# Kernel optimization log

Hardware: AMD Instinct MI355X
Metric: run time of the kernel (lower is better)

Reference implementation:

```python
import jax, jax.numpy as jnp
import numpy as np

S, L, E = 64, 256, 768          # sentences, tokens per sentence, BERT hidden
N, P = 4096, 32768              # events, event pairs
C, H, D = 256, 4, 64            # CGE channels, heads, head dim (C = H*D = n_last)
M = 8                           # max event span length
MLP_H = 1024
ITERS = 3                       # max_iteration + 1
RATE = 0.5
BETA_INTRA, BETA_INTER = 0.5, 0.5


def setup_inputs():
    key = jax.random.key(0)
    ks = jax.random.split(key, 16)
    nrm = lambda k, shape, sc: jax.random.normal(k, shape, dtype=jnp.float32) * sc
    event_start = jax.random.randint(ks[2], (N,), 0, L - M)
    span = jax.random.randint(ks[3], (N,), 1, M + 1)
    return {
        "sent_emb": nrm(ks[0], (S, L, E), 1.0),
        "proj_in_W": nrm(ks[7], (E, C), E ** -0.5),
        "proj_in_b": jnp.zeros((C,), jnp.float32),
        "proj_W": nrm(ks[8], (C, C), C ** -0.5),
        "proj_b": jnp.zeros((C,), jnp.float32),
        "att_src_intra": nrm(ks[9], (H, D), D ** -0.5),
        "att_dst_intra": nrm(ks[10], (H, D), D ** -0.5),
        "att_src_inter": nrm(ks[11], (H, D), D ** -0.5),
        "att_dst_inter": nrm(ks[12], (H, D), D ** -0.5),
        "mlp_W1": nrm(ks[13], (C + 2 * E, MLP_H), (C + 2 * E) ** -0.5),
        "mlp_b1": jnp.zeros((MLP_H,), jnp.float32),
        "mlp_W2": nrm(ks[14], (MLP_H, 3), MLP_H ** -0.5),
        "mlp_b2": jnp.zeros((3,), jnp.float32),
        "event_sent": jax.random.randint(ks[1], (N,), 0, S),
        "event_start": event_start,
        "event_end": event_start + span,
        "pair_idx": jax.random.randint(ks[4], (P, 2), 0, N),
        "rel_type": jax.random.randint(ks[5], (P,), 0, 2),
        "target": jax.random.randint(ks[6], (P,), 0, 3),
    }


def _attend(h, src, dst, emask, att_src, att_dst):
    # h: [N,H,D]. Masked graph attention, softmax over incoming edges per dst.
    a = jax.nn.leaky_relu((h[src] * att_src).sum(-1) + (h[dst] * att_dst).sum(-1), 0.2)  # [En,H]
    a = jnp.where(emask[:, None], a, -1e9)
    amax = jnp.maximum(jax.ops.segment_max(a, dst, num_segments=N), -1e9)  # [N,H]
    ex = jnp.exp(a - amax[dst]) * emask[:, None].astype(a.dtype)
    denom = jax.ops.segment_sum(ex, dst, num_segments=N)
    alpha = ex / (denom[dst] + 1e-9)
    out = jax.ops.segment_sum(alpha[:, :, None] * h[src], dst, num_segments=N)  # [N,H,D]
    return out.reshape(N, H * D)


def _forward(sent_emb, proj_in_W, proj_in_b, proj_W, proj_b,
             att_src_intra, att_dst_intra, att_src_inter, att_dst_inter,
             mlp_W1, mlp_b1, mlp_W2, mlp_b2,
             event_sent, event_start, event_end, pair_idx, rel_type, target):
    # extract_event: mean of sentence token embeddings over each event span
    pos = event_start[:, None] + jnp.arange(M)                      # [N,M]
    vmask = (pos < event_end[:, None]).astype(sent_emb.dtype)       # [N,M]
    tok = sent_emb[event_sent[:, None], jnp.clip(pos, 0, L - 1)]    # [N,M,E]
    e_emb = (tok * vmask[..., None]).sum(1) / (event_end - event_start).astype(sent_emb.dtype)[:, None]

    p0, p1 = pair_idx[:, 0], pair_idx[:, 1]
    pair_emb = jnp.concatenate([e_emb[p0], e_emb[p1]], axis=-1)     # [P,2E]
    x = e_emb @ proj_in_W + proj_in_b                               # [N,C]

    self_idx = jnp.arange(N)
    ones_n = jnp.ones((N,), bool)
    src_all = jnp.concatenate([p0, p1])
    dst_all = jnp.concatenate([p1, p0])
    intra2 = jnp.concatenate([rel_type == 0, rel_type == 0])

    loss = jnp.float32(0.0)
    pred = None
    for it in range(ITERS):
        diff = x[p0] - x[p1]                                        # [P,C]
        pre = jnp.concatenate([pair_emb, diff], axis=-1)            # [P,2E+C]
        pred = jax.nn.relu(pre @ mlp_W1 + mlp_b1) @ mlp_W2 + mlp_b2  # [P,3]
        logp = jax.nn.log_softmax(pred, axis=-1)
        loss = loss + (1.0 / (it + 1)) * (-jnp.take_along_axis(logp, target[:, None], axis=1).mean())

        # data-dependent edge construction (masked, fixed-size edge lists)
        psoft = jax.nn.softmax(pred, axis=-1)
        conf = psoft.max(1) > RATE
        parg = psoft.argmax(1)
        m_all = jnp.concatenate([conf & (parg == 1), conf & (parg == 2)])

        h = (x @ proj_W + proj_b).reshape(N, H, D)
        # intra edges + always-on self loops
        src_i = jnp.concatenate([src_all, self_idx])
        dst_i = jnp.concatenate([dst_all, self_idx])
        m_i = jnp.concatenate([m_all & intra2, ones_n])
        out_intra = _attend(h, src_i, dst_i, m_i, att_src_intra, att_dst_intra)
        out_inter = _attend(h, src_all, dst_all, m_all & (~intra2), att_src_inter, att_dst_inter)
        x = BETA_INTRA * out_intra + BETA_INTER * out_inter
    return loss, pred


def reference(sent_emb, proj_in_W, proj_in_b, proj_W, proj_b,
              att_src_intra, att_dst_intra, att_src_inter, att_dst_inter,
              mlp_W1, mlp_b1, mlp_W2, mlp_b2,
              event_sent, event_start, event_end, pair_idx, rel_type, target):
    return _forward(sent_emb, proj_in_W, proj_in_b, proj_W, proj_b,
                    att_src_intra, att_dst_intra, att_src_inter, att_dst_inter,
                    mlp_W1, mlp_b1, mlp_W2, mlp_b2,
                    event_sent, event_start, event_end, pair_idx, rel_type, target)
```

## Files before the change

kernel.cpp:

```cpp
#include <hip/hip_runtime.h>
#include <cstddef>
#include <cstdint>

#define NEV   4096
#define NPAIR 32768
#define NEDGE (2*NPAIR)
#define EDIM  768
#define CDIM  256
#define MLPH  1024
#define LLEN  256

typedef unsigned short u16;
typedef __attribute__((ext_vector_type(8))) short bhalf8;
typedef __attribute__((ext_vector_type(4))) float f32x4;

#define GLOAD_LDS(g, l) __builtin_amdgcn_global_load_lds( \
    (const __attribute__((address_space(1))) unsigned int*)(g), \
    (__attribute__((address_space(3))) unsigned int*)(l), 16, 0, 0)

__device__ inline u16 f2bf(float f) {
  union { float f; unsigned u; } v; v.f = f;
  unsigned r = v.u + 0x7fffu + ((v.u >> 16) & 1u);
  return (u16)(r >> 16);
}
__device__ inline float bf2f(u16 h) {
  union { unsigned u; float f; } v; v.u = ((unsigned)h) << 16; return v.f;
}

__global__ void k_zero(int* __restrict__ deg, int* __restrict__ pdeg,
                       float* __restrict__ out) {
  int i = blockIdx.x * 256 + threadIdx.x;
  if (i < NEV) { deg[i] = 0; pdeg[i] = 0; }
  if (i == 0) out[0] = 0.f;
}

__global__ void k_embed(const float* __restrict__ sent, const int* __restrict__ es,
                        const int* __restrict__ st, const int* __restrict__ en,
                        u16* __restrict__ Ahat) {
  int node = blockIdx.x;
  int s = es[node];
  int a = st[node];
  int span = en[node] - a;
  float fspan = (float)span;
  const float* base = sent + ((size_t)s * LLEN + a) * EDIM;
  for (int d = threadIdx.x; d < EDIM; d += 256) {
    float acc = 0.f;
    for (int m = 0; m < span; ++m) acc += base[(size_t)m * EDIM + d];
    float e = acc / fspan;
    u16 hi = f2bf(e);
    float lo = e - bf2f(hi);
    size_t b = (size_t)node * (3 * EDIM);
    Ahat[b + d] = hi;
    Ahat[b + EDIM + d] = hi;
    Ahat[b + 2 * EDIM + d] = f2bf(lo);
  }
}

__global__ void k_countF(const int* __restrict__ pair, int* __restrict__ deg,
                         int* __restrict__ pdeg) {
  int e = blockIdx.x * 256 + threadIdx.x;
  if (e >= NEDGE) return;
  int p = (e < NPAIR) ? e : e - NPAIR;
  int dst = (e < NPAIR) ? pair[2 * p + 1] : pair[2 * p];
  atomicAdd(&deg[dst], 1);
  if (e < NPAIR) atomicAdd(&pdeg[pair[2 * e]], 1);
}

__device__ inline void scan_body(const int* __restrict__ deg, int* __restrict__ rowp,
                                 int* __restrict__ cursor, int* part) {
  int t = threadIdx.x;
  int base = t * 16;
  int sum = 0;
  for (int i = 0; i < 16; ++i) sum += deg[base + i];
  part[t] = sum;
  __syncthreads();
  for (int off = 1; off < 256; off <<= 1) {
    int v = (t >= off) ? part[t - off] : 0;
    __syncthreads();
    part[t] += v;
    __syncthreads();
  }
  int run = (t == 0) ? 0 : part[t - 1];
  for (int i = 0; i < 16; ++i) {
    rowp[base + i] = run;
    cursor[base + i] = 0;
    run += deg[base + i];
  }
  if (t == 255) rowp[NEV] = run;
}

__global__ void k_scanF(const int* __restrict__ deg, int* __restrict__ rowp,
                        int* __restrict__ cursor, const int* __restrict__ pdeg,
                        int* __restrict__ prow, int* __restrict__ pcur) {
  __shared__ int part[256];
  scan_body(deg, rowp, cursor, part);
  __syncthreads();
  scan_body(pdeg, prow, pcur, part);
}

__global__ void k_scatterF(const int* __restrict__ pair, const int* __restrict__ rowp,
                           int* __restrict__ cursor, int* __restrict__ e_src,
                           int* __restrict__ e_id, const int* __restrict__ prow,
                           int* __restrict__ pcur, int* __restrict__ pidx) {
  int e = blockIdx.x * 256 + threadIdx.x;
  if (e >= NEDGE) return;
  int p   = (e < NPAIR) ? e : e - NPAIR;
  int src = (e < NPAIR) ? pair[2 * p]     : pair[2 * p + 1];
  int dst = (e < NPAIR) ? pair[2 * p + 1] : pair[2 * p];
  int pos = rowp[dst] + atomicAdd(&cursor[dst], 1);
  e_src[pos] = src;
  e_id[pos]  = e;
  if (e < NPAIR) {
    int pp = prow[pair[2 * e]] + atomicAdd(&pcur[pair[2 * e]], 1);
    pidx[pp] = e;
  }
}

__global__ __launch_bounds__(256) void cvt_w(const float* __restrict__ W1,
                                             const float* __restrict__ piW,
                                             const float* __restrict__ projW,
                                             u16* __restrict__ BTe,
                                             u16* __restrict__ BTu)
{
  __shared__ float tile[32][33];
  int which = (blockIdx.y >= 24) ? 1 : 0;
  if (which && blockIdx.x >= 40) return;
  u16* BT = which ? BTu : BTe;
  int K = which ? CDIM : EDIM;
  int ld = K * 3;
  int bk = (which ? (blockIdx.y - 24) : blockIdx.y) * 32;
  int bc = blockIdx.x * 32;
  int tx = threadIdx.x & 31, ty = threadIdx.x >> 5;
#pragma unroll
  for (int rr = 0; rr < 4; ++rr) {
    int k = bk + ty + rr * 8;
    int c = bc + tx;
    float v;
    if (which == 0) {
      v = (c < 1024) ? W1[(size_t)k * MLPH + c]
        : (c < 2048) ? W1[(size_t)(EDIM + k) * MLPH + (c - 1024)]
        : piW[(size_t)k * CDIM + (c - 2048)];
    } else {
      v = (c < 1024) ? W1[(size_t)(2 * EDIM + k) * MLPH + c]
        : projW[(size_t)k * CDIM + (c - 1024)];
    }
    tile[ty + rr * 8][tx] = v;
  }
  __syncthreads();
#pragma unroll
  for (int rr = 0; rr < 4; ++rr) {
    int c = bc + ty + rr * 8;
    int k = bk + tx;
    float v = tile[tx][ty + rr * 8];
    u16 hi = f2bf(v);
    float lo = v - bf2f(hi);
    size_t b = (size_t)c * ld;
    BT[b + k] = hi;
    BT[b + K + k] = f2bf(lo);
    BT[b + 2 * K + k] = hi;
  }
}

__global__ __launch_bounds__(256) void mgemm(
    const u16* __restrict__ A, const u16* __restrict__ BT, int Kp, int mode,
    float* __restrict__ G1, float* __restrict__ G2, u16* __restrict__ Xhat,
    const float* __restrict__ pib, const float* __restrict__ b1,
    const float* __restrict__ pb, float* __restrict__ U, float* __restrict__ V,
    float* __restrict__ h, const float* __restrict__ asi,
    const float* __restrict__ adi, const float* __restrict__ asj,
    const float* __restrict__ adj, float* __restrict__ sv)
{
  __shared__ u16 As[64 * 64];
  __shared__ u16 Bs[128 * 64];
  int tid = threadIdx.x;
  int wave = tid >> 6, lane = tid & 63;

  int gx = gridDim.x;
  int nwg = gx * gridDim.y;
  int orig = blockIdx.y * gx + blockIdx.x;
  int swz = (orig & 7) * (nwg >> 3) + (orig >> 3);
  int bm = (swz / gx) * 64, bn = (swz % gx) * 128;

  int wm = (wave >> 1) * 32, wn = (wave & 1) * 64;

  int srow = tid >> 3;
  int scol = (tid & 7) << 3;
  const u16* Ag = A + (size_t)(bm + srow) * Kp + scol;
  const u16* Bg = BT + (size_t)(bn + srow) * Kp + scol;
  u16* Asd = &As[tid * 8];
  u16* Bsd = &Bs[tid * 8];

  f32x4 acc[2][4];
#pragma unroll
  for (int i = 0; i < 2; ++i)
#pragma unroll
    for (int j = 0; j < 4; ++j) {
      f32x4 z = {0.f, 0.f, 0.f, 0.f};
      acc[i][j] = z;
    }

  int fr = lane & 15;
  int fq = lane >> 4;

  for (int k0 = 0; k0 < Kp; k0 += 64) {
#pragma unroll
    for (int c = 0; c < 2; ++c)
      GLOAD_LDS(Ag + (size_t)(c * 32) * Kp, Asd + c * 2048);
#pragma unroll
    for (int c = 0; c < 4; ++c)
      GLOAD_LDS(Bg + (size_t)(c * 32) * Kp, Bsd + c * 2048);
    __syncthreads();
#pragma unroll
    for (int kk = 0; kk < 2; ++kk) {
      bhalf8 af[2], bf[4];
#pragma unroll
      for (int i = 0; i < 2; ++i)
        af[i] = *(const bhalf8*)&As[(wm + i * 16 + fr) * 64 + kk * 32 + fq * 8];
#pragma unroll
      for (int j = 0; j < 4; ++j)
        bf[j] = *(const bhalf8*)&Bs[(wn + j * 16 + fr) * 64 + kk * 32 + fq * 8];
#pragma unroll
      for (int i = 0; i < 2; ++i)
#pragma unroll
        for (int j = 0; j < 4; ++j)
          acc[i][j] = __builtin_amdgcn_mfma_f32_16x16x32_bf16(af[i], bf[j], acc[i][j], 0, 0, 0);
    }
    __syncthreads();
    Ag += 64;
    Bg += 64;
  }

#pragma unroll
  for (int i = 0; i < 2; ++i) {
    int mrow = bm + wm + i * 16 + fq * 4;
#pragma unroll
    for (int g = 0; g < 4; ++g) {
      int m = mrow + g;
#pragma unroll
      for (int j = 0; j < 4; ++j) {
        int c = bn + wn + j * 16 + fr;
        float vv = acc[i][j][g];
        if (mode == 0) {
          if (c < 1024) {
            G1[(size_t)m * MLPH + c] = vv;
          } else if (c < 2048) {
            G2[(size_t)m * MLPH + (c - 1024)] = vv;
          } else {
            int cc = c - 2048;
            float xv = vv + pib[cc];
            u16 hi = f2bf(xv);
            float lo = xv - bf2f(hi);
            size_t b = (size_t)m * (3 * CDIM);
            Xhat[b + cc] = hi;
            Xhat[b + CDIM + cc] = hi;
            Xhat[b + 2 * CDIM + cc] = f2bf(lo);
          }
        } else {
          if (c < 1024) {
            size_t idx = (size_t)m * MLPH + c;
            U[idx] = G1[idx] + vv + b1[c];
            V[idx] = G2[idx] - vv;
          } else {
            int cc = c - 1024;
            h[(size_t)m * CDIM + cc] = vv + pb[cc];
          }
        }
      }
    }
  }

  if (mode == 1 && bn >= MLPH) {
    int hbase = bn - MLPH + wn;
    int head = hbase >> 6;
#pragma unroll
    for (int i = 0; i < 2; ++i) {
#pragma unroll
      for (int g = 0; g < 4; ++g) {
        int m = bm + wm + i * 16 + fq * 4 + g;
        float p0 = 0.f, p1 = 0.f, p2 = 0.f, p3 = 0.f;
#pragma unroll
        for (int j = 0; j < 4; ++j) {
          int hc = hbase + j * 16 + fr;
          float hv = acc[i][j][g] + pb[hc];
          p0 += hv * asi[hc];
          p1 += hv * adi[hc];
          p2 += hv * asj[hc];
          p3 += hv * adj[hc];
        }
#pragma unroll
        for (int mm = 1; mm < 16; mm <<= 1) {
          p0 += __shfl_xor(p0, mm);
          p1 += __shfl_xor(p1, mm);
          p2 += __shfl_xor(p2, mm);
          p3 += __shfl_xor(p3, mm);
        }
        if (fr == 0) {
          sv[0 * NEV * 4 + m * 4 + head] = p0;
          sv[1 * NEV * 4 + m * 4 + head] = p1;
          sv[2 * NEV * 4 + m * 4 + head] = p2;
          sv[3 * NEV * 4 + m * 4 + head] = p3;
        }
      }
    }
  }
}

__global__ __launch_bounds__(256) void k_pred_g(
    const float* __restrict__ U, const float* __restrict__ V,
    const int* __restrict__ pair, const int* __restrict__ prow,
    const int* __restrict__ pidx, const float* __restrict__ W2,
    const float* __restrict__ b2, const int* __restrict__ target,
    int* __restrict__ mstate, float* __restrict__ out,
    float* __restrict__ partials, float lossCoef)
{
  __shared__ float ush[MLPH];
  __shared__ float red[4];
  int n = blockIdx.x;
  int tid = threadIdx.x;
  const float* u = U + (size_t)n * MLPH;
#pragma unroll
  for (int i = 0; i < 4; ++i) ush[tid + i * 256] = u[tid + i * 256];
  __syncthreads();
  int wv = tid >> 6, lane = tid & 63;
  int beg = prow[n], end = prow[n + 1];
  float lsum = 0.f;
  for (int ip = beg + wv; ip < end; ip += 4) {
    int p = pidx[ip];
    int i1 = pair[2 * p + 1];
    const float* v = V + (size_t)i1 * MLPH;
    float a0 = 0.f, a1 = 0.f, a2 = 0.f;
    for (int kb = (lane << 2); kb < MLPH; kb += 256) {
      float4 uu = *(const float4*)(&ush[kb]);
      float4 vv = *(const float4*)(v + kb);
      float h0 = fmaxf(uu.x + vv.x, 0.f);
      float h1 = fmaxf(uu.y + vv.y, 0.f);
      float h2 = fmaxf(uu.z + vv.z, 0.f);
      float h3 = fmaxf(uu.w + vv.w, 0.f);
      const float4* w4 = (const float4*)(W2 + 3 * kb);
      float4 wa = w4[0], wb = w4[1], wc = w4[2];
      a0 += h0 * wa.x + h1 * wa.w + h2 * wb.z + h3 * wc.y;
      a1 += h0 * wa.y + h1 * wb.x + h2 * wb.w + h3 * wc.z;
      a2 += h0 * wa.z + h1 * wb.y + h2 * wc.x + h3 * wc.w;
    }
#pragma unroll
    for (int m = 32; m >= 1; m >>= 1) {
      a0 += __shfl_down(a0, m);
      a1 += __shfl_down(a1, m);
      a2 += __shfl_down(a2, m);
    }
    if (lane == 0) {
      a0 += b2[0]; a1 += b2[1]; a2 += b2[2];
      float mx = fmaxf(a0, fmaxf(a1, a2));
      float e0 = expf(a0 - mx), e1 = expf(a1 - mx), e2 = expf(a2 - mx);
      float sum = e0 + e1 + e2;
      int arg = 0; float best = e0;
      if (e1 > best) { best = e1; arg = 1; }
      if (e2 > best) { best = e2; arg = 2; }
      bool conf = (best / sum) > 0.5f;
      mstate[p] = conf ? arg : -1;
      int t = target[p];
      float predt = (t == 0) ? a0 : ((t == 1) ? a1 : a2);
      float logp = (predt - mx) - logf(sum);
      lsum += -logp * lossCoef;
      float* po = out + 1 + (size_t)p * 3;
      po[0] = a0; po[1] = a1; po[2] = a2;
    }
  }
  if (lane == 0) red[wv] = lsum;
  __syncthreads();
  if (tid == 0) partials[n] = red[0] + red[1] + red[2] + red[3];
}

__global__ __launch_bounds__(256) void k_attn(
    const float* __restrict__ h, const float* __restrict__ sv,
    const int* __restrict__ rowp, const int* __restrict__ e_src,
    const int* __restrict__ e_id, const int* __restrict__ mstate,
    const int* __restrict__ rel, u16* __restrict__ Xhat,
    const float* __restrict__ lpart, float* __restrict__ out)
{
  int node = blockIdx.x;
  int t = threadIdx.x;
  int head = t >> 6;
  const float* s_si = sv;
  const float* s_di = sv + NEV * 4;
  const float* s_sj = sv + 2 * NEV * 4;
  const float* s_dj = sv + 3 * NEV * 4;
  float sdi = s_di[node * 4 + head];
  float sdj = s_dj[node * 4 + head];
  int beg = rowp[node], end = rowp[node + 1];
  float aself = s_si[node * 4 + head] + sdi;
  aself = aself > 0.f ? aself : 0.2f * aself;
  float mxi = aself;
  float mxj = -1e9f;
  for (int e = beg; e < end; ++e) {
    int eid = e_id[e];
    int pp = (eid < NPAIR) ? eid : eid - NPAIR;
    int st = mstate[pp];
    bool mall = (eid < NPAIR) ? (st == 1) : (st == 2);
    if (!mall) continue;
    int src = e_src[e];
    if (rel[pp] == 0) {
      float a = s_si[src * 4 + head] + sdi;
      a = a > 0.f ? a : 0.2f * a;
      mxi = fmaxf(mxi, a);
    } else {
      float a = s_sj[src * 4 + head] + sdj;
      a = a > 0.f ? a : 0.2f * a;
      mxj = fmaxf(mxj, a);
    }
  }
  float deni = 0.f, denj = 0.f, acci = 0.f, accj = 0.f;
  {
    float ex = expf(aself - mxi);
    deni += ex;
    acci += ex * h[(size_t)node * CDIM + t];
  }
  for (int e = beg; e < end; ++e) {
    int eid = e_id[e];
    int pp = (eid < NPAIR) ? eid : eid - NPAIR;
    int st = mstate[pp];
    bool mall = (eid < NPAIR) ? (st == 1) : (st == 2);
    if (!mall) continue;
    int src = e_src[e];
    float hval = h[(size_t)src * CDIM + t];
    if (rel[pp] == 0) {
      float a = s_si[src * 4 + head] + sdi;
      a = a > 0.f ? a : 0.2f * a;
      float ex = expf(a - mxi);
      deni += ex; acci += ex * hval;
    } else {
      float a = s_sj[src * 4 + head] + sdj;
      a = a > 0.f ? a : 0.2f * a;
      float ex = expf(a - mxj);
      denj += ex; accj += ex * hval;
    }
  }
  float outv = 0.5f * (acci / (deni + 1e-9f)) + 0.5f * (accj / (denj + 1e-9f));
  u16 hi = f2bf(outv);
  float lo = outv - bf2f(hi);
  size_t b = (size_t)node * (3 * CDIM);
  Xhat[b + t] = hi;
  Xhat[b + CDIM + t] = hi;
  Xhat[b + 2 * CDIM + t] = f2bf(lo);

  if (blockIdx.x == 0) {
    __shared__ float sm[256];
    float s = 0.f;
    for (int i = t; i < NEV; i += 256) s += lpart[i];
    sm[t] = s;
    __syncthreads();
    for (int off = 128; off; off >>= 1) {
      if (t < off) sm[t] += sm[t + off];
      __syncthreads();
    }
    if (t == 0) out[0] += sm[0];
  }
}

extern "C" void kernel_launch(void* const* d_in, const int* in_sizes, int n_in,
                              void* d_out, int out_size, void* d_ws, size_t ws_size,
                              hipStream_t stream)
{
  const float* sent      = (const float*)d_in[0];
  const float* proj_in_W = (const float*)d_in[1];
  const float* proj_in_b = (const float*)d_in[2];
  const float* proj_W    = (const float*)d_in[3];
  const float* proj_b    = (const float*)d_in[4];
  const float* asi       = (const float*)d_in[5];
  const float* adi       = (const float*)d_in[6];
  const float* asj       = (const float*)d_in[7];
  const float* adj       = (const float*)d_in[8];
  const float* W1        = (const float*)d_in[9];
  const float* b1        = (const float*)d_in[10];
  const float* W2        = (const float*)d_in[11];
  const float* b2        = (const float*)d_in[12];
  const int*   es        = (const int*)d_in[13];
  const int*   st        = (const int*)d_in[14];
  const int*   en        = (const int*)d_in[15];
  const int*   pair      = (const int*)d_in[16];
  const int*   rel       = (const int*)d_in[17];
  const int*   target    = (const int*)d_in[18];
  float* out = (float*)d_out;

  char* w = (char*)d_ws;
  auto alloc = [&](size_t bytes) -> char* {
    char* p = w;
    w += (bytes + 255) & ~(size_t)255;
    return p;
  };
  u16*   Ahat = (u16*)alloc(sizeof(u16) * (size_t)NEV * 3 * EDIM);
  u16*   BTe  = (u16*)alloc(sizeof(u16) * (size_t)2304 * 2304);
  u16*   BTu  = (u16*)alloc(sizeof(u16) * (size_t)1280 * 768);
  u16*   Xhat = (u16*)alloc(sizeof(u16) * (size_t)NEV * 3 * CDIM);
  float* G1   = (float*)alloc(sizeof(float) * (size_t)NEV * MLPH);
  float* G2   = (float*)alloc(sizeof(float) * (size_t)NEV * MLPH);
  float* U    = (float*)alloc(sizeof(float) * (size_t)NEV * MLPH);
  float* V    = (float*)alloc(sizeof(float) * (size_t)NEV * MLPH);
  float* h    = (float*)alloc(sizeof(float) * (size_t)NEV * CDIM);
  float* sv   = (float*)alloc(sizeof(float) * (size_t)NEV * 16);
  float* lpart= (float*)alloc(sizeof(float) * NEV);
  int* deg    = (int*)alloc(sizeof(int) * NEV);
  int* rowp   = (int*)alloc(sizeof(int) * (NEV + 1));
  int* cursor = (int*)alloc(sizeof(int) * NEV);
  int* e_src  = (int*)alloc(sizeof(int) * NEDGE);
  int* e_id   = (int*)alloc(sizeof(int) * NEDGE);
  int* pdeg   = (int*)alloc(sizeof(int) * NEV);
  int* prow   = (int*)alloc(sizeof(int) * (NEV + 1));
  int* pcur   = (int*)alloc(sizeof(int) * NEV);
  int* pidx   = (int*)alloc(sizeof(int) * NPAIR);
  int* mstate = (int*)alloc(sizeof(int) * NPAIR);

  k_zero<<<(NEV + 255) / 256, 256, 0, stream>>>(deg, pdeg, out);
  k_embed<<<NEV, 256, 0, stream>>>(sent, es, st, en, Ahat);
  k_countF<<<NEDGE / 256, 256, 0, stream>>>(pair, deg, pdeg);
  k_scanF<<<1, 256, 0, stream>>>(deg, rowp, cursor, pdeg, prow, pcur);
  k_scatterF<<<NEDGE / 256, 256, 0, stream>>>(pair, rowp, cursor, e_src, e_id,
                                              prow, pcur, pidx);
  cvt_w<<<dim3(72, 32), 256, 0, stream>>>(W1, proj_in_W, proj_W, BTe, BTu);

  mgemm<<<dim3(2304 / 128, NEV / 64), 256, 0, stream>>>(
      Ahat, BTe, 3 * EDIM, 0, G1, G2, Xhat, proj_in_b,
      nullptr, nullptr, nullptr, nullptr, nullptr,
      nullptr, nullptr, nullptr, nullptr, nullptr);

  for (int it = 0; it < 3; ++it) {
    mgemm<<<dim3(1280 / 128, NEV / 64), 256, 0, stream>>>(
        Xhat, BTu, 3 * CDIM, 1, G1, G2, nullptr, nullptr,
        b1, proj_b, U, V, h, asi, adi, asj, adj, sv);
    float coef = 1.0f / ((float)(it + 1) * (float)NPAIR);
    k_pred_g<<<NEV, 256, 0, stream>>>(U, V, pair, prow, pidx, W2, b2, target,
                                      mstate, out, lpart, coef);
    k_attn<<<NEV, 256, 0, stream>>>(h, sv, rowp, e_src, e_id, mstate, rel, Xhat,
                                    lpart, out);
  }
  (void)in_sizes; (void)n_in; (void)out_size; (void)ws_size;
}
```

Before: 544.3 us.

## Store split-bf16 operands as hi/lo pairs and issue three MFMAs per tile

Drops the duplicated hi block from the split-bf16 operand layout, so A and B are stored as [hi|lo] (2K) instead of [hi|hi|lo] (3K). The GEMM now loads hi and lo tiles separately into LDS and issues hi*hi, hi*lo and lo*hi MFMAs explicitly. This cuts global memory traffic and workspace for the embedding, weight and Xhat operands while keeping the MFMA count the same. It also removes the workgroup swizzle, which may hurt L2 locality, and halves the K-step to 32 so there are more barriers per unit of work.

```diff
diff --git a/kernel.cpp b/kernel.cpp
--- a/kernel.cpp
+++ b/kernel.cpp
@@ -49,10 +49,9 @@
     float e = acc / fspan;
     u16 hi = f2bf(e);
     float lo = e - bf2f(hi);
-    size_t b = (size_t)node * (3 * EDIM);
+    size_t b = (size_t)node * (2 * EDIM);
     Ahat[b + d] = hi;
-    Ahat[b + EDIM + d] = hi;
-    Ahat[b + 2 * EDIM + d] = f2bf(lo);
+    Ahat[b + EDIM + d] = f2bf(lo);
   }
 }
 
@@ -127,7 +126,7 @@
   if (which && blockIdx.x >= 40) return;
   u16* BT = which ? BTu : BTe;
   int K = which ? CDIM : EDIM;
-  int ld = K * 3;
+  int ld = K * 2;
   int bk = (which ? (blockIdx.y - 24) : blockIdx.y) * 32;
   int bc = blockIdx.x * 32;
   int tx = threadIdx.x & 31, ty = threadIdx.x >> 5;
@@ -157,12 +156,11 @@
     size_t b = (size_t)c * ld;
     BT[b + k] = hi;
     BT[b + K + k] = f2bf(lo);
-    BT[b + 2 * K + k] = hi;
   }
 }
 
 __global__ __launch_bounds__(256) void mgemm(
-    const u16* __restrict__ A, const u16* __restrict__ BT, int Kp, int mode,
+    const u16* __restrict__ A, const u16* __restrict__ BT, int K, int mode,
     float* __restrict__ G1, float* __restrict__ G2, u16* __restrict__ Xhat,
     const float* __restrict__ pib, const float* __restrict__ b1,
     const float* __restrict__ pb, float* __restrict__ U, float* __restrict__ V,
@@ -170,25 +168,21 @@
     const float* __restrict__ adi, const float* __restrict__ asj,
     const float* __restrict__ adj, float* __restrict__ sv)
 {
-  __shared__ u16 As[64 * 64];
-  __shared__ u16 Bs[128 * 64];
+  __shared__ u16 Ash[64 * 32];
+  __shared__ u16 Asl[64 * 32];
+  __shared__ u16 Bsh[128 * 32];
+  __shared__ u16 Bsl[128 * 32];
   int tid = threadIdx.x;
   int wave = tid >> 6, lane = tid & 63;
-
-  int gx = gridDim.x;
-  int nwg = gx * gridDim.y;
-  int orig = blockIdx.y * gx + blockIdx.x;
-  int swz = (orig & 7) * (nwg >> 3) + (orig >> 3);
-  int bm = (swz / gx) * 64, bn = (swz % gx) * 128;
-
+  int bm = blockIdx.y * 64, bn = blockIdx.x * 128;
   int wm = (wave >> 1) * 32, wn = (wave & 1) * 64;
 
-  int srow = tid >> 3;
-  int scol = (tid & 7) << 3;
-  const u16* Ag = A + (size_t)(bm + srow) * Kp + scol;
-  const u16* Bg = BT + (size_t)(bn + srow) * Kp + scol;
-  u16* Asd = &As[tid * 8];
-  u16* Bsd = &Bs[tid * 8];
+  int Kp2 = 2 * K;
+  int srow = tid >> 2;
+  int scol = (tid & 3) << 3;
+  const u16* AgH = A + (size_t)(bm + srow) * Kp2 + scol;
+  const u16* BgH = BT + (size_t)(bn + srow) * Kp2 + scol;
+  const u16* BgH2 = BT + (size_t)(bn + 64 + srow) * Kp2 + scol;
 
   f32x4 acc[2][4];
 #pragma unroll
@@ -202,32 +196,34 @@
   int fr = lane & 15;
   int fq = lane >> 4;
 
-  for (int k0 = 0; k0 < Kp; k0 += 64) {
-#pragma unroll
-    for (int c = 0; c < 2; ++c)
-      GLOAD_LDS(Ag + (size_t)(c * 32) * Kp, Asd + c * 2048);
-#pragma unroll
-    for (int c = 0; c < 4; ++c)
-      GLOAD_LDS(Bg + (size_t)(c * 32) * Kp, Bsd + c * 2048);
+  for (int kc = 0; kc < K; kc += 32) {
+    GLOAD_LDS(AgH + kc,       &Ash[tid * 8]);
+    GLOAD_LDS(AgH + K + kc,   &Asl[tid * 8]);
+    GLOAD_LDS(BgH + kc,       &Bsh[tid * 8]);
+    GLOAD_LDS(BgH2 + kc,      &Bsh[2048 + tid * 8]);
+    GLOAD_LDS(BgH + K + kc,   &Bsl[tid * 8]);
+    GLOAD_LDS(BgH2 + K + kc,  &Bsl[2048 + tid * 8]);
     __syncthreads();
-#pragma unroll
-    for (int kk = 0; kk < 2; ++kk) {
-      bhalf8 af[2], bf[4];
-#pragma unroll
-      for (int i = 0; i < 2; ++i)
-        af[i] = *(const bhalf8*)&As[(wm + i * 16 + fr) * 64 + kk * 32 + fq * 8];
-#pragma unroll
-      for (int j = 0; j < 4; ++j)
-        bf[j] = *(const bhalf8*)&Bs[(wn + j * 16 + fr) * 64 + kk * 32 + fq * 8];
-#pragma unroll
-      for (int i = 0; i < 2; ++i)
-#pragma unroll
-        for (int j = 0; j < 4; ++j)
-          acc[i][j] = __builtin_amdgcn_mfma_f32_16x16x32_bf16(af[i], bf[j], acc[i][j], 0, 0, 0);
-    }
+    bhalf8 afh[2], afl[2], bfh[4], bfl[4];
+#pragma unroll
+    for (int i = 0; i < 2; ++i) {
+      afh[i] = *(const bhalf8*)&Ash[(wm + i * 16 + fr) * 32 + fq * 8];
+      afl[i] = *(const bhalf8*)&Asl[(wm + i * 16 + fr) * 32 + fq * 8];
+    }
+#pragma unroll
+    for (int j = 0; j < 4; ++j) {
+      bfh[j] = *(const bhalf8*)&Bsh[(wn + j * 16 + fr) * 32 + fq * 8];
+      bfl[j] = *(const bhalf8*)&Bsl[(wn + j * 16 + fr) * 32 + fq * 8];
+    }
+#pragma unroll
+    for (int i = 0; i < 2; ++i)
+#pragma unroll
+      for (int j = 0; j < 4; ++j) {
+        acc[i][j] = __builtin_amdgcn_mfma_f32_16x16x32_bf16(afh[i], bfh[j], acc[i][j], 0, 0, 0);
+        acc[i][j] = __builtin_amdgcn_mfma_f32_16x16x32_bf16(afh[i], bfl[j], acc[i][j], 0, 0, 0);
+        acc[i][j] = __builtin_amdgcn_mfma_f32_16x16x32_bf16(afl[i], bfh[j], acc[i][j], 0, 0, 0);
+      }
     __syncthreads();
-    Ag += 64;
-    Bg += 64;
   }
 
 #pragma unroll
@@ -250,10 +246,9 @@
             float xv = vv + pib[cc];
             u16 hi = f2bf(xv);
             float lo = xv - bf2f(hi);
-            size_t b = (size_t)m * (3 * CDIM);
+            size_t b = (size_t)m * (2 * CDIM);
             Xhat[b + cc] = hi;
-            Xhat[b + CDIM + cc] = hi;
-            Xhat[b + 2 * CDIM + cc] = f2bf(lo);
+            Xhat[b + CDIM + cc] = f2bf(lo);
           }
         } else {
           if (c < 1024) {
@@ -438,10 +433,9 @@
   float outv = 0.5f * (acci / (deni + 1e-9f)) + 0.5f * (accj / (denj + 1e-9f));
   u16 hi = f2bf(outv);
   float lo = outv - bf2f(hi);
-  size_t b = (size_t)node * (3 * CDIM);
+  size_t b = (size_t)node * (2 * CDIM);
   Xhat[b + t] = hi;
-  Xhat[b + CDIM + t] = hi;
-  Xhat[b + 2 * CDIM + t] = f2bf(lo);
+  Xhat[b + CDIM + t] = f2bf(lo);
 
   if (blockIdx.x == 0) {
     __shared__ float sm[256];
@@ -488,10 +482,10 @@
     w += (bytes + 255) & ~(size_t)255;
     return p;
   };
-  u16*   Ahat = (u16*)alloc(sizeof(u16) * (size_t)NEV * 3 * EDIM);
-  u16*   BTe  = (u16*)alloc(sizeof(u16) * (size_t)2304 * 2304);
-  u16*   BTu  = (u16*)alloc(sizeof(u16) * (size_t)1280 * 768);
-  u16*   Xhat = (u16*)alloc(sizeof(u16) * (size_t)NEV * 3 * CDIM);
+  u16*   Ahat = (u16*)alloc(sizeof(u16) * (size_t)NEV * 2 * EDIM);
+  u16*   BTe  = (u16*)alloc(sizeof(u16) * (size_t)2304 * 1536);
+  u16*   BTu  = (u16*)alloc(sizeof(u16) * (size_t)1280 * 512);
+  u16*   Xhat = (u16*)alloc(sizeof(u16) * (size_t)NEV * 2 * CDIM);
   float* G1   = (float*)alloc(sizeof(float) * (size_t)NEV * MLPH);
   float* G2   = (float*)alloc(sizeof(float) * (size_t)NEV * MLPH);
   float* U    = (float*)alloc(sizeof(float) * (size_t)NEV * MLPH);
@@ -519,13 +513,13 @@
   cvt_w<<<dim3(72, 32), 256, 0, stream>>>(W1, proj_in_W, proj_W, BTe, BTu);
 
   mgemm<<<dim3(2304 / 128, NEV / 64), 256, 0, stream>>>(
-      Ahat, BTe, 3 * EDIM, 0, G1, G2, Xhat, proj_in_b,
+      Ahat, BTe, EDIM, 0, G1, G2, Xhat, proj_in_b,
       nullptr, nullptr, nullptr, nullptr, nullptr,
       nullptr, nullptr, nullptr, nullptr, nullptr);
 
   for (int it = 0; it < 3; ++it) {
     mgemm<<<dim3(1280 / 128, NEV / 64), 256, 0, stream>>>(
-        Xhat, BTu, 3 * CDIM, 1, G1, G2, nullptr, nullptr,
+        Xhat, BTu, CDIM, 1, G1, G2, nullptr, nullptr,
         b1, proj_b, U, V, h, asi, adi, asj, adj, sv);
     float coef = 1.0f / ((float)(it + 1) * (float)NPAIR);
     k_pred_g<<<NEV, 256, 0, stream>>>(U, V, pair, prow, pidx, W2, b2, target,
```

After: 503.8 us. 1.08x faster.
